# Performance work log

Measured on AMD Instinct MI355X. Metric: run time of the kernel, lower is better.

The kernel has to match this reference:

```python
import jax, jax.numpy as jnp
import numpy as np

B, T, C = 4, 2048, 1024
H, D = 16, 64  # num_heads, head_size; H*D == C


def setup_inputs() -> dict:
    key = jax.random.key(0)
    ks = jax.random.split(key, 6)
    s = C ** -0.5
    return {
        "x": jax.random.normal(ks[0], (B, T, C), dtype=jnp.float32),
        "Wq": jax.random.normal(ks[1], (H, C, D), dtype=jnp.float32) * s,
        "Wk": jax.random.normal(ks[2], (H, C, D), dtype=jnp.float32) * s,
        "Wv": jax.random.normal(ks[3], (H, C, D), dtype=jnp.float32) * s,
        "Wo": jax.random.normal(ks[4], (C, C), dtype=jnp.float32) * s,
        "bo": jnp.zeros((C,), dtype=jnp.float32),
    }


def reference(x, Wq, Wk, Wv, Wo, bo):
    # Per-head projections, vectorized over heads: [B,T,C] x [H,C,D] -> [B,H,T,D]
    q = jnp.einsum("btc,hcd->bhtd", x, Wq)
    k = jnp.einsum("btc,hcd->bhtd", x, Wk)
    v = jnp.einsum("btc,hcd->bhtd", x, Wv)
    # NOTE: original scales by n_embd**-0.5 (input channel C), not head_size.
    scale = jnp.asarray(C, x.dtype) ** -0.5
    scores = jnp.einsum("bhtd,bhsd->bhts", q, k) * scale  # [B,H,T,T]
    causal = jnp.tril(jnp.ones((T, T), dtype=bool))
    scores = jnp.where(causal, scores, jnp.asarray(-jnp.inf, x.dtype))
    attn = jax.nn.softmax(scores, axis=-1)
    out = jnp.einsum("bhts,bhsd->bhtd", attn, v)  # [B,H,T,D]
    # concat heads: [B,T,H*D] == [B,T,C]
    out = out.transpose(0, 2, 1, 3).reshape(B, T, H * D)
    return out @ Wo.T + bo
```

## Files before the change

kernel.cpp:

```cpp
#include <hip/hip_runtime.h>
#include <hip/hip_bf16.h>
#include <math.h>

#define B_ 4
#define T_ 2048
#define C_ 1024
#define H_ 16
#define D_ 64
#define BT (B_*T_)
#define BH (B_*H_)

typedef __bf16 bf16x8 __attribute__((ext_vector_type(8)));
typedef __bf16 bf16x4 __attribute__((ext_vector_type(4)));
typedef float f32x4 __attribute__((ext_vector_type(4)));
typedef unsigned short u16;
typedef u16 u16x8 __attribute__((ext_vector_type(8)));

#define GLL(g, l) __builtin_amdgcn_global_load_lds( \
    (const __attribute__((address_space(1))) unsigned int*)(g), \
    (__attribute__((address_space(3))) unsigned int*)(l), 16, 0, 0)

#define SCALE2 0.04508422f

#define SBAR()   do { asm volatile("" ::: "memory"); __builtin_amdgcn_s_barrier(); asm volatile("" ::: "memory"); } while (0)
#define WAITV(n) asm volatile("s_waitcnt vmcnt(" #n ")" ::: "memory")

__device__ __forceinline__ u16 f2b(float f) {
    union { float f; unsigned u; } v; v.f = f;
    unsigned r = v.u + 0x7fffu + ((v.u >> 16) & 1u);
    return (u16)(r >> 16);
}

__global__ __launch_bounds__(256) void prep(const float* __restrict__ x,
                                            const float* __restrict__ Wo,
                                            const float* __restrict__ Wq,
                                            const float* __restrict__ Wk,
                                            const float* __restrict__ Wv,
                                            u16* __restrict__ xbf,
                                            u16* __restrict__ wobf,
                                            u16* __restrict__ wt) {
    __shared__ u16 lds[64][72];
    int bid = blockIdx.x, tid = threadIdx.x;
    if (bid < 8192) {
        int g = bid * 256 + tid;
        float4 v = ((const float4*)x)[g];
        ushort4 o;
        o.x = f2b(v.x); o.y = f2b(v.y); o.z = f2b(v.z); o.w = f2b(v.w);
        ((ushort4*)xbf)[g] = o;
        return;
    }
    if (bid < 9216) {
        int g = (bid - 8192) * 256 + tid;
        float4 v = ((const float4*)Wo)[g];
        ushort4 o;
        o.x = f2b(v.x); o.y = f2b(v.y); o.z = f2b(v.z); o.w = f2b(v.w);
        ((ushort4*)wobf)[g] = o;
        return;
    }
    int id = bid - 9216;
    int cb = id & 15, h = (id >> 4) & 15, w = id >> 8;
    const float* W = (w == 0) ? Wq : (w == 1) ? Wk : Wv;
    float sc = (w == 0) ? SCALE2 : 1.0f;
    int c0 = cb * 64;
    {
        int col = (tid & 15) * 4;
        for (int cc = 0; cc < 4; ++cc) {
            int r = (tid >> 4) + cc * 16;
            float4 v = *(const float4*)&W[(size_t)(h * C_ + c0 + r) * D_ + col];
            lds[r][col + 0] = f2b(v.x * sc); lds[r][col + 1] = f2b(v.y * sc);
            lds[r][col + 2] = f2b(v.z * sc); lds[r][col + 3] = f2b(v.w * sc);
        }
    }
    __syncthreads();
    {
        int tcol = (tid & 7) * 8;
        for (int cc = 0; cc < 2; ++cc) {
            int d = (tid >> 3) + cc * 32;
            u16x8 t;
            for (int j = 0; j < 8; ++j) t[j] = lds[tcol + j][d];
            *(u16x8*)&wt[(((size_t)(w * H_ + h) * D_ + d) * C_) + c0 + tcol] = t;
        }
    }
}

__global__ __launch_bounds__(256) void qkv_gemm(const u16* __restrict__ xbf,
                                                const u16* __restrict__ wt,
                                                u16* __restrict__ q, u16* __restrict__ k,
                                                u16* __restrict__ vt) {
    __shared__ u16 Al[128][64];
    __shared__ u16 Bl[128][64];
    int mb = blockIdx.x, nb = blockIdx.y;
    int tid = threadIdx.x, wv = tid >> 6, lane = tid & 63, l15 = lane & 15, quad = lane >> 4;
    int rowh = (wv & 1) * 64, colh = (wv >> 1) * 64;
    f32x4 acc[4][4];
    #pragma unroll
    for (int i = 0; i < 4; ++i)
        #pragma unroll
        for (int j = 0; j < 4; ++j) acc[i][j] = (f32x4){0.f, 0.f, 0.f, 0.f};
    int lrow = lane >> 3;
    int srow = wv * 32 + lrow;
    int scol = (((lane & 7) ^ lrow)) * 8;
    const u16* agp = &xbf[(size_t)(mb * 128 + srow) * C_ + scol];
    const u16* bgp = &wt[(size_t)(nb * 128 + srow) * C_ + scol];
    int rsw = l15 & 7;
    for (int k0 = 0; k0 < C_; k0 += 64) {
        #pragma unroll
        for (int j = 0; j < 4; ++j) {
            GLL(agp + (size_t)(j * 8) * C_ + k0, &Al[wv * 32 + j * 8][0]);
            GLL(bgp + (size_t)(j * 8) * C_ + k0, &Bl[wv * 32 + j * 8][0]);
        }
        __syncthreads();
        #pragma unroll
        for (int ks = 0; ks < 2; ++ks) {
            int cbl = (((ks << 2) | quad) ^ rsw) * 8;
            bf16x8 af[4], bf[4];
            #pragma unroll
            for (int mt = 0; mt < 4; ++mt)
                af[mt] = *(const bf16x8*)&Al[rowh + mt * 16 + l15][cbl];
            #pragma unroll
            for (int nt = 0; nt < 4; ++nt)
                bf[nt] = *(const bf16x8*)&Bl[colh + nt * 16 + l15][cbl];
            #pragma unroll
            for (int mt = 0; mt < 4; ++mt)
                #pragma unroll
                for (int nt = 0; nt < 4; ++nt)
                    acc[mt][nt] = __builtin_amdgcn_mfma_f32_16x16x32_bf16(af[mt], bf[nt], acc[mt][nt], 0, 0, 0);
        }
        __syncthreads();
    }
    int bb = (mb * 128) >> 11;
    #pragma unroll
    for (int nt = 0; nt < 4; ++nt) {
        int n0 = nb * 128 + colh + nt * 16;
        int wsel = n0 >> 10, hh = (n0 >> 6) & 15, d0 = n0 & 63;
        if (wsel == 2) {
            u16* vrow = vt + ((size_t)((bb * H_ + hh) * D_) + d0 + l15) * T_;
            #pragma unroll
            for (int mt = 0; mt < 4; ++mt) {
                int tbase = ((mb * 128 + rowh + mt * 16) & (T_ - 1)) + quad * 4;
                bf16x4 w;
                #pragma unroll
                for (int r = 0; r < 4; ++r) w[r] = (__bf16)acc[mt][nt][r];
                *(bf16x4*)&vrow[tbase] = w;
            }
        } else {
            u16* op = (wsel == 0) ? q : k;
            #pragma unroll
            for (int mt = 0; mt < 4; ++mt)
                #pragma unroll
                for (int r = 0; r < 4; ++r) {
                    int m = mb * 128 + rowh + mt * 16 + quad * 4 + r;
                    int tt = m & (T_ - 1);
                    op[((size_t)(bb * H_ + hh) * T_ + tt) * D_ + d0 + l15] = f2b(acc[mt][nt][r]);
                }
        }
    }
}

__global__ __launch_bounds__(256, 2) void attn(const u16* __restrict__ q, const u16* __restrict__ kk,
                                               const u16* __restrict__ vt, u16* __restrict__ att) {
    __shared__ u16 Kl[2][64][64];
    __shared__ u16 Vl[2][64][64];
    __shared__ u16 Pl[4][32][72];
    int bh = blockIdx.x, c = 15 - blockIdx.y;
    int b = bh >> 4, h = bh & 15;
    int tid = threadIdx.x, wid = tid >> 6, lane = tid & 63, l15 = lane & 15, quad = lane >> 4;
    const u16* qbase = q + (size_t)bh * T_ * D_;
    const u16* kbase = kk + (size_t)bh * T_ * D_;
    const u16* vbase = vt + (size_t)bh * D_ * T_;
    u16* pw = &Pl[wid][0][0];
    bf16x8 ones;
    #pragma unroll
    for (int j = 0; j < 8; ++j) ones[j] = (__bf16)1.0f;
    int r8 = lane >> 3;
    int csrc = ((lane & 7) ^ r8) * 8;
    int strow = wid * 16 + r8;
    int rsw = l15 & 7;

    int R0q = c * 128 + wid * 32;
    int ktb = 2 * c + 1;
    int kmax_w = R0q >> 6;
    bf16x8 bq[2][2];
    #pragma unroll
    for (int qt = 0; qt < 2; ++qt)
        #pragma unroll
        for (int kd = 0; kd < 2; ++kd)
            bq[qt][kd] = *(const bf16x8*)&qbase[(size_t)(R0q + qt * 16 + l15) * D_ + kd * 32 + quad * 8];
    f32x4 o[4][2];
    f32x4 lacc[2];
    #pragma unroll
    for (int dt = 0; dt < 4; ++dt)
        #pragma unroll
        for (int qt = 0; qt < 2; ++qt) o[dt][qt] = (f32x4){0.f, 0.f, 0.f, 0.f};
    lacc[0] = (f32x4){0.f, 0.f, 0.f, 0.f};
    lacc[1] = (f32x4){0.f, 0.f, 0.f, 0.f};
    #pragma unroll
    for (int j = 0; j < 2; ++j) {
        GLL(kbase + (size_t)(strow + j * 8) * D_ + csrc, &Kl[0][wid * 16 + j * 8][0]);
        GLL(vbase + (size_t)(strow + j * 8) * T_ + csrc, &Vl[0][wid * 16 + j * 8][0]);
    }
    for (int kt = 0; kt <= ktb; ++kt) {
        int cur = kt & 1;
        if (kt < ktb) {
            int kn = (kt + 1) * 64;
            #pragma unroll
            for (int j = 0; j < 2; ++j) {
                GLL(kbase + (size_t)(kn + strow + j * 8) * D_ + csrc, &Kl[cur ^ 1][wid * 16 + j * 8][0]);
                GLL(vbase + (size_t)(strow + j * 8) * T_ + kn + csrc, &Vl[cur ^ 1][wid * 16 + j * 8][0]);
            }
            WAITV(4);
        } else {
            WAITV(0);
        }
        SBAR();
        if (kt <= kmax_w) {
            int k0 = kt * 64;
            f32x4 sS[4][2];
            #pragma unroll
            for (int kvt = 0; kvt < 4; ++kvt)
                #pragma unroll
                for (int qt = 0; qt < 2; ++qt) sS[kvt][qt] = (f32x4){0.f, 0.f, 0.f, 0.f};
            #pragma unroll
            for (int kd = 0; kd < 2; ++kd) {
                int cblk = (((kd << 2) | quad) ^ rsw) * 8;
                bf16x8 akf[4];
                #pragma unroll
                for (int kvt = 0; kvt < 4; ++kvt)
                    akf[kvt] = *(const bf16x8*)&Kl[cur][kvt * 16 + l15][cblk];
                #pragma unroll
                for (int kvt = 0; kvt < 4; ++kvt)
                    #pragma unroll
                    for (int qt = 0; qt < 2; ++qt)
                        sS[kvt][qt] = __builtin_amdgcn_mfma_f32_16x16x32_bf16(akf[kvt], bq[qt][kd], sS[kvt][qt], 0, 0, 0);
            }
            if (kt == kmax_w) {
                #pragma unroll
                for (int qt = 0; qt < 2; ++qt) {
                    int qabs = R0q + qt * 16 + l15;
                    #pragma unroll
                    for (int kvt = 0; kvt < 4; ++kvt) {
                        int kvb = k0 + kvt * 16 + quad * 4;
                        #pragma unroll
                        for (int r = 0; r < 4; ++r)
                            if (kvb + r > qabs) sS[kvt][qt][r] = -INFINITY;
                    }
                }
            }
            #pragma unroll
            for (int kvt = 0; kvt < 4; ++kvt)
                #pragma unroll
                for (int qt = 0; qt < 2; ++qt)
                    #pragma unroll
                    for (int r = 0; r < 4; ++r)
                        sS[kvt][qt][r] = __builtin_amdgcn_exp2f(sS[kvt][qt][r]);
            #pragma unroll
            for (int qt = 0; qt < 2; ++qt)
                #pragma unroll
                for (int kvt = 0; kvt < 4; ++kvt) {
                    bf16x4 w;
                    #pragma unroll
                    for (int r = 0; r < 4; ++r) w[r] = (__bf16)sS[kvt][qt][r];
                    *(bf16x4*)&pw[(qt * 16 + l15) * 72 + kvt * 16 + quad * 4] = w;
                }
            #pragma unroll
            for (int ks = 0; ks < 2; ++ks) {
                int cblk = (((ks << 2) | quad) ^ rsw) * 8;
                bf16x8 avf[4];
                #pragma unroll
                for (int dt = 0; dt < 4; ++dt)
                    avf[dt] = *(const bf16x8*)&Vl[cur][dt * 16 + l15][cblk];
                #pragma unroll
                for (int qt = 0; qt < 2; ++qt) {
                    bf16x8 bp = *(const bf16x8*)&pw[(qt * 16 + l15) * 72 + ks * 32 + quad * 8];
                    #pragma unroll
                    for (int dt = 0; dt < 4; ++dt)
                        o[dt][qt] = __builtin_amdgcn_mfma_f32_16x16x32_bf16(avf[dt], bp, o[dt][qt], 0, 0, 0);
                    lacc[qt] = __builtin_amdgcn_mfma_f32_16x16x32_bf16(ones, bp, lacc[qt], 0, 0, 0);
                }
            }
        }
        SBAR();
    }
    #pragma unroll
    for (int qt = 0; qt < 2; ++qt) {
        float rl = __builtin_amdgcn_rcpf(lacc[qt][0]);
        int qabs = R0q + qt * 16 + l15;
        #pragma unroll
        for (int dt = 0; dt < 4; ++dt) {
            bf16x4 w;
            #pragma unroll
            for (int r = 0; r < 4; ++r) w[r] = (__bf16)(o[dt][qt][r] * rl);
            *(bf16x4*)&att[(size_t)(b * T_ + qabs) * C_ + h * 64 + dt * 16 + quad * 4] = w;
        }
    }
}

__global__ __launch_bounds__(256) void out_gemm(const u16* __restrict__ att,
                                                const u16* __restrict__ wo,
                                                const float* __restrict__ bo,
                                                float* __restrict__ out) {
    __shared__ u16 Al[128][64];
    __shared__ u16 Bl[128][64];
    int mb = blockIdx.x, nb = blockIdx.y;
    int tid = threadIdx.x, wv = tid >> 6, lane = tid & 63, l15 = lane & 15, quad = lane >> 4;
    int rowh = (wv & 1) * 64, colh = (wv >> 1) * 64;
    f32x4 acc[4][4];
    #pragma unroll
    for (int i = 0; i < 4; ++i)
        #pragma unroll
        for (int j = 0; j < 4; ++j) acc[i][j] = (f32x4){0.f, 0.f, 0.f, 0.f};
    int lrow = lane >> 3;
    int srow = wv * 32 + lrow;
    int scol = (((lane & 7) ^ lrow)) * 8;
    const u16* agp = &att[(size_t)(mb * 128 + srow) * C_ + scol];
    const u16* bgp = &wo[(size_t)(nb * 128 + srow) * C_ + scol];
    int rsw = l15 & 7;
    for (int k0 = 0; k0 < C_; k0 += 64) {
        #pragma unroll
        for (int j = 0; j < 4; ++j) {
            GLL(agp + (size_t)(j * 8) * C_ + k0, &Al[wv * 32 + j * 8][0]);
            GLL(bgp + (size_t)(j * 8) * C_ + k0, &Bl[wv * 32 + j * 8][0]);
        }
        __syncthreads();
        #pragma unroll
        for (int ks = 0; ks < 2; ++ks) {
            int cbl = (((ks << 2) | quad) ^ rsw) * 8;
            bf16x8 af[4], bf[4];
            #pragma unroll
            for (int mt = 0; mt < 4; ++mt)
                af[mt] = *(const bf16x8*)&Al[rowh + mt * 16 + l15][cbl];
            #pragma unroll
            for (int nt = 0; nt < 4; ++nt)
                bf[nt] = *(const bf16x8*)&Bl[colh + nt * 16 + l15][cbl];
            #pragma unroll
            for (int mt = 0; mt < 4; ++mt)
                #pragma unroll
                for (int nt = 0; nt < 4; ++nt)
                    acc[mt][nt] = __builtin_amdgcn_mfma_f32_16x16x32_bf16(af[mt], bf[nt], acc[mt][nt], 0, 0, 0);
        }
        __syncthreads();
    }
    #pragma unroll
    for (int nt = 0; nt < 4; ++nt) {
        int n = nb * 128 + colh + nt * 16 + l15;
        float bias = bo[n];
        #pragma unroll
        for (int mt = 0; mt < 4; ++mt)
            #pragma unroll
            for (int r = 0; r < 4; ++r) {
                int m = mb * 128 + rowh + mt * 16 + quad * 4 + r;
                out[(size_t)m * C_ + n] = acc[mt][nt][r] + bias;
            }
    }
}

extern "C" void kernel_launch(void* const* d_in, const int* in_sizes, int n_in,
                              void* d_out, int out_size, void* d_ws, size_t ws_size,
                              hipStream_t stream) {
    const float* x  = (const float*)d_in[0];
    const float* Wq = (const float*)d_in[1];
    const float* Wk = (const float*)d_in[2];
    const float* Wv = (const float*)d_in[3];
    const float* Wo = (const float*)d_in[4];
    const float* bo = (const float*)d_in[5];
    float* out = (float*)d_out;
    char* ws = (char*)d_ws;
    u16* xbf  = (u16*)(ws + (size_t)0);
    u16* wt   = (u16*)(ws + ((size_t)16 << 20));
    u16* wobf = (u16*)(ws + ((size_t)22 << 20));
    u16* qb   = (u16*)(ws + ((size_t)24 << 20));
    u16* kb   = (u16*)(ws + ((size_t)40 << 20));
    u16* vtb  = (u16*)(ws + ((size_t)56 << 20));
    u16* attb = (u16*)(ws + ((size_t)72 << 20));

    hipLaunchKernelGGL(prep, dim3(9984), dim3(256), 0, stream, x, Wo, Wq, Wk, Wv, xbf, wobf, wt);
    hipLaunchKernelGGL(qkv_gemm, dim3(BT / 128, 3 * C_ / 128), dim3(256), 0, stream, xbf, wt, qb, kb, vtb);
    hipLaunchKernelGGL(attn, dim3(BH, 16), dim3(256), 0, stream, qb, kb, vtb, attb);
    hipLaunchKernelGGL(out_gemm, dim3(BT / 128, C_ / 128), dim3(256), 0, stream, attb, wobf, bo, out);
}
```

Baseline: 225.0 us.

## Fuse all four stages into one persistent kernel with grid barriers

```diff
diff --git a/kernel.cpp b/kernel.cpp
--- a/kernel.cpp
+++ b/kernel.cpp
@@ -9,6 +9,7 @@
 #define D_ 64
 #define BT (B_*T_)
 #define BH (B_*H_)
+#define NBLK 512u
 
 typedef __bf16 bf16x8 __attribute__((ext_vector_type(8)));
 typedef __bf16 bf16x4 __attribute__((ext_vector_type(4)));
@@ -31,326 +32,341 @@
     return (u16)(r >> 16);
 }
 
-__global__ __launch_bounds__(256) void prep(const float* __restrict__ x,
-                                            const float* __restrict__ Wo,
-                                            const float* __restrict__ Wq,
-                                            const float* __restrict__ Wk,
-                                            const float* __restrict__ Wv,
-                                            u16* __restrict__ xbf,
-                                            u16* __restrict__ wobf,
-                                            u16* __restrict__ wt) {
-    __shared__ u16 lds[64][72];
+__device__ __forceinline__ void gridbar(unsigned* cnt, int idx) {
+    __syncthreads();
+    if (threadIdx.x == 0) {
+        __threadfence();
+        atomicAdd(&cnt[idx], 1u);
+        while (__hip_atomic_load(&cnt[idx], __ATOMIC_RELAXED, __HIP_MEMORY_SCOPE_AGENT) < NBLK)
+            __builtin_amdgcn_s_sleep(2);
+        __threadfence();
+    }
+    __syncthreads();
+}
+
+union SMem {
+    struct { u16 Al[128][64]; u16 Bl[128][64]; } g;
+    struct { u16 Kl[2][64][64]; u16 Vl[2][64][64]; u16 Pl[4][32][72]; } a;
+    u16 p[64][72];
+};
+
+__global__ __launch_bounds__(256, 2) void fused(
+    const float* __restrict__ x,
+    const float* __restrict__ Wq, const float* __restrict__ Wk,
+    const float* __restrict__ Wv, const float* __restrict__ Wo,
+    const float* __restrict__ bo,
+    u16* __restrict__ xbf, u16* __restrict__ wobf, u16* __restrict__ wt,
+    u16* __restrict__ qb, u16* __restrict__ kb, u16* __restrict__ vtb,
+    u16* __restrict__ attb, float* __restrict__ out, unsigned* __restrict__ bar)
+{
+    __shared__ SMem sm;
     int bid = blockIdx.x, tid = threadIdx.x;
-    if (bid < 8192) {
-        int g = bid * 256 + tid;
-        float4 v = ((const float4*)x)[g];
-        ushort4 o;
-        o.x = f2b(v.x); o.y = f2b(v.y); o.z = f2b(v.z); o.w = f2b(v.w);
-        ((ushort4*)xbf)[g] = o;
-        return;
-    }
-    if (bid < 9216) {
-        int g = (bid - 8192) * 256 + tid;
-        float4 v = ((const float4*)Wo)[g];
-        ushort4 o;
-        o.x = f2b(v.x); o.y = f2b(v.y); o.z = f2b(v.z); o.w = f2b(v.w);
-        ((ushort4*)wobf)[g] = o;
-        return;
-    }
-    int id = bid - 9216;
-    int cb = id & 15, h = (id >> 4) & 15, w = id >> 8;
-    const float* W = (w == 0) ? Wq : (w == 1) ? Wk : Wv;
-    float sc = (w == 0) ? SCALE2 : 1.0f;
-    int c0 = cb * 64;
+    int lane = tid & 63, l15 = lane & 15, quad = lane >> 4;
+    int wv = tid >> 6;
+
+    for (int u = bid; u < 9984; u += 512) {
+        if (u < 8192) {
+            int g = u * 256 + tid;
+            float4 v = ((const float4*)x)[g];
+            ushort4 o4;
+            o4.x = f2b(v.x); o4.y = f2b(v.y); o4.z = f2b(v.z); o4.w = f2b(v.w);
+            ((ushort4*)xbf)[g] = o4;
+        } else if (u < 9216) {
+            int g = (u - 8192) * 256 + tid;
+            float4 v = ((const float4*)Wo)[g];
+            ushort4 o4;
+            o4.x = f2b(v.x); o4.y = f2b(v.y); o4.z = f2b(v.z); o4.w = f2b(v.w);
+            ((ushort4*)wobf)[g] = o4;
+        } else {
+            int id = u - 9216;
+            int cb = id & 15, h = (id >> 4) & 15, w = id >> 8;
+            const float* W = (w == 0) ? Wq : (w == 1) ? Wk : Wv;
+            float sc = (w == 0) ? SCALE2 : 1.0f;
+            int c0 = cb * 64;
+            {
+                int col = (tid & 15) * 4;
+                for (int cc = 0; cc < 4; ++cc) {
+                    int r = (tid >> 4) + cc * 16;
+                    float4 v = *(const float4*)&W[(size_t)(h * C_ + c0 + r) * D_ + col];
+                    sm.p[r][col + 0] = f2b(v.x * sc); sm.p[r][col + 1] = f2b(v.y * sc);
+                    sm.p[r][col + 2] = f2b(v.z * sc); sm.p[r][col + 3] = f2b(v.w * sc);
+                }
+            }
+            __syncthreads();
+            {
+                int tcol = (tid & 7) * 8;
+                for (int cc = 0; cc < 2; ++cc) {
+                    int d = (tid >> 3) + cc * 32;
+                    u16x8 t;
+                    for (int j = 0; j < 8; ++j) t[j] = sm.p[tcol + j][d];
+                    *(u16x8*)&wt[(((size_t)(w * H_ + h) * D_ + d) * C_) + c0 + tcol] = t;
+                }
+            }
+            __syncthreads();
+        }
+    }
+    gridbar(bar, 0);
+
     {
-        int col = (tid & 15) * 4;
-        for (int cc = 0; cc < 4; ++cc) {
-            int r = (tid >> 4) + cc * 16;
-            float4 v = *(const float4*)&W[(size_t)(h * C_ + c0 + r) * D_ + col];
-            lds[r][col + 0] = f2b(v.x * sc); lds[r][col + 1] = f2b(v.y * sc);
-            lds[r][col + 2] = f2b(v.z * sc); lds[r][col + 3] = f2b(v.w * sc);
-        }
-    }
-    __syncthreads();
+        int rowh = (wv & 1) * 64, colh = (wv >> 1) * 64;
+        int lrow = lane >> 3;
+        int srow = wv * 32 + lrow;
+        int scol = ((lane & 7) ^ lrow) * 8;
+        int rsw = l15 & 7;
+        for (int i = 0; i < 3; ++i) {
+            int u = bid + 512 * i;
+            int mb = u & 63, nb = u >> 6;
+            f32x4 acc[4][4];
+            #pragma unroll
+            for (int a1 = 0; a1 < 4; ++a1)
+                #pragma unroll
+                for (int a2 = 0; a2 < 4; ++a2) acc[a1][a2] = (f32x4){0.f, 0.f, 0.f, 0.f};
+            const u16* agp = &xbf[(size_t)(mb * 128 + srow) * C_ + scol];
+            const u16* bgp = &wt[(size_t)(nb * 128 + srow) * C_ + scol];
+            for (int k0 = 0; k0 < C_; k0 += 64) {
+                #pragma unroll
+                for (int j = 0; j < 4; ++j) {
+                    GLL(agp + (size_t)(j * 8) * C_ + k0, &sm.g.Al[wv * 32 + j * 8][0]);
+                    GLL(bgp + (size_t)(j * 8) * C_ + k0, &sm.g.Bl[wv * 32 + j * 8][0]);
+                }
+                __syncthreads();
+                #pragma unroll
+                for (int ks = 0; ks < 2; ++ks) {
+                    int cbl = (((ks << 2) | quad) ^ rsw) * 8;
+                    bf16x8 af[4], bf[4];
+                    #pragma unroll
+                    for (int mt = 0; mt < 4; ++mt)
+                        af[mt] = *(const bf16x8*)&sm.g.Al[rowh + mt * 16 + l15][cbl];
+                    #pragma unroll
+                    for (int nt = 0; nt < 4; ++nt)
+                        bf[nt] = *(const bf16x8*)&sm.g.Bl[colh + nt * 16 + l15][cbl];
+                    #pragma unroll
+                    for (int mt = 0; mt < 4; ++mt)
+                        #pragma unroll
+                        for (int nt = 0; nt < 4; ++nt)
+                            acc[mt][nt] = __builtin_amdgcn_mfma_f32_16x16x32_bf16(af[mt], bf[nt], acc[mt][nt], 0, 0, 0);
+                }
+                __syncthreads();
+            }
+            int bb = (mb * 128) >> 11;
+            #pragma unroll
+            for (int nt = 0; nt < 4; ++nt) {
+                int n0 = nb * 128 + colh + nt * 16;
+                int wsel = n0 >> 10, hh = (n0 >> 6) & 15, d0 = n0 & 63;
+                if (wsel == 2) {
+                    u16* vrow = vtb + ((size_t)((bb * H_ + hh) * D_) + d0 + l15) * T_;
+                    #pragma unroll
+                    for (int mt = 0; mt < 4; ++mt) {
+                        int tbase = ((mb * 128 + rowh + mt * 16) & (T_ - 1)) + quad * 4;
+                        bf16x4 w;
+                        #pragma unroll
+                        for (int r = 0; r < 4; ++r) w[r] = (__bf16)acc[mt][nt][r];
+                        *(bf16x4*)&vrow[tbase] = w;
+                    }
+                } else {
+                    u16* op = (wsel == 0) ? qb : kb;
+                    #pragma unroll
+                    for (int mt = 0; mt < 4; ++mt)
+                        #pragma unroll
+                        for (int r = 0; r < 4; ++r) {
+                            int m = mb * 128 + rowh + mt * 16 + quad * 4 + r;
+                            int tt = m & (T_ - 1);
+                            op[((size_t)(bb * H_ + hh) * T_ + tt) * D_ + d0 + l15] = f2b(acc[mt][nt][r]);
+                        }
+                }
+            }
+        }
+    }
+    gridbar(bar, 1);
+
     {
-        int tcol = (tid & 7) * 8;
-        for (int cc = 0; cc < 2; ++cc) {
-            int d = (tid >> 3) + cc * 32;
-            u16x8 t;
-            for (int j = 0; j < 8; ++j) t[j] = lds[tcol + j][d];
-            *(u16x8*)&wt[(((size_t)(w * H_ + h) * D_ + d) * C_) + c0 + tcol] = t;
-        }
-    }
-}
-
-__global__ __launch_bounds__(256) void qkv_gemm(const u16* __restrict__ xbf,
-                                                const u16* __restrict__ wt,
-                                                u16* __restrict__ q, u16* __restrict__ k,
-                                                u16* __restrict__ vt) {
-    __shared__ u16 Al[128][64];
-    __shared__ u16 Bl[128][64];
-    int mb = blockIdx.x, nb = blockIdx.y;
-    int tid = threadIdx.x, wv = tid >> 6, lane = tid & 63, l15 = lane & 15, quad = lane >> 4;
-    int rowh = (wv & 1) * 64, colh = (wv >> 1) * 64;
-    f32x4 acc[4][4];
-    #pragma unroll
-    for (int i = 0; i < 4; ++i)
+        int wid = wv;
+        int bh = bid & 63, y = bid >> 6;
+        int b = bh >> 4, h = bh & 15;
+        const u16* qbase = qb + (size_t)bh * T_ * D_;
+        const u16* kbase = kb + (size_t)bh * T_ * D_;
+        const u16* vbase = vtb + (size_t)bh * D_ * T_;
+        u16* pw = &sm.a.Pl[wid][0][0];
+        bf16x8 ones;
         #pragma unroll
-        for (int j = 0; j < 4; ++j) acc[i][j] = (f32x4){0.f, 0.f, 0.f, 0.f};
-    int lrow = lane >> 3;
-    int srow = wv * 32 + lrow;
-    int scol = (((lane & 7) ^ lrow)) * 8;
-    const u16* agp = &xbf[(size_t)(mb * 128 + srow) * C_ + scol];
-    const u16* bgp = &wt[(size_t)(nb * 128 + srow) * C_ + scol];
-    int rsw = l15 & 7;
-    for (int k0 = 0; k0 < C_; k0 += 64) {
+        for (int j = 0; j < 8; ++j) ones[j] = (__bf16)1.0f;
+        int r8 = lane >> 3;
+        int csrc = ((lane & 7) ^ r8) * 8;
+        int strow = wid * 16 + r8;
+        int rsw = l15 & 7;
+        for (int p = 0; p < 2; ++p) {
+            int c = p ? y : 15 - y;
+            int R0q = c * 128 + wid * 32;
+            int ktb = 2 * c + 1;
+            int kmax_w = R0q >> 6;
+            bf16x8 bq[2][2];
+            #pragma unroll
+            for (int qt = 0; qt < 2; ++qt)
+                #pragma unroll
+                for (int kd = 0; kd < 2; ++kd)
+                    bq[qt][kd] = *(const bf16x8*)&qbase[(size_t)(R0q + qt * 16 + l15) * D_ + kd * 32 + quad * 8];
+            f32x4 o[4][2];
+            f32x4 lacc[2];
+            #pragma unroll
+            for (int dt = 0; dt < 4; ++dt)
+                #pragma unroll
+                for (int qt = 0; qt < 2; ++qt) o[dt][qt] = (f32x4){0.f, 0.f, 0.f, 0.f};
+            lacc[0] = (f32x4){0.f, 0.f, 0.f, 0.f};
+            lacc[1] = (f32x4){0.f, 0.f, 0.f, 0.f};
+            #pragma unroll
+            for (int j = 0; j < 2; ++j) {
+                GLL(kbase + (size_t)(strow + j * 8) * D_ + csrc, &sm.a.Kl[0][wid * 16 + j * 8][0]);
+                GLL(vbase + (size_t)(strow + j * 8) * T_ + csrc, &sm.a.Vl[0][wid * 16 + j * 8][0]);
+            }
+            for (int kt = 0; kt <= ktb; ++kt) {
+                int cur = kt & 1;
+                if (kt < ktb) {
+                    int kn = (kt + 1) * 64;
+                    #pragma unroll
+                    for (int j = 0; j < 2; ++j) {
+                        GLL(kbase + (size_t)(kn + strow + j * 8) * D_ + csrc, &sm.a.Kl[cur ^ 1][wid * 16 + j * 8][0]);
+                        GLL(vbase + (size_t)(strow + j * 8) * T_ + kn + csrc, &sm.a.Vl[cur ^ 1][wid * 16 + j * 8][0]);
+                    }
+                    WAITV(4);
+                } else {
+                    WAITV(0);
+                }
+                SBAR();
+                if (kt <= kmax_w) {
+                    int k0 = kt * 64;
+                    f32x4 sS[4][2];
+                    #pragma unroll
+                    for (int kvt = 0; kvt < 4; ++kvt)
+                        #pragma unroll
+                        for (int qt = 0; qt < 2; ++qt) sS[kvt][qt] = (f32x4){0.f, 0.f, 0.f, 0.f};
+                    #pragma unroll
+                    for (int kd = 0; kd < 2; ++kd) {
+                        int cblk = (((kd << 2) | quad) ^ rsw) * 8;
+                        bf16x8 akf[4];
+                        #pragma unroll
+                        for (int kvt = 0; kvt < 4; ++kvt)
+                            akf[kvt] = *(const bf16x8*)&sm.a.Kl[cur][kvt * 16 + l15][cblk];
+                        #pragma unroll
+                        for (int kvt = 0; kvt < 4; ++kvt)
+                            #pragma unroll
+                            for (int qt = 0; qt < 2; ++qt)
+                                sS[kvt][qt] = __builtin_amdgcn_mfma_f32_16x16x32_bf16(akf[kvt], bq[qt][kd], sS[kvt][qt], 0, 0, 0);
+                    }
+                    if (kt == kmax_w) {
+                        #pragma unroll
+                        for (int qt = 0; qt < 2; ++qt) {
+                            int qabs = R0q + qt * 16 + l15;
+                            #pragma unroll
+                            for (int kvt = 0; kvt < 4; ++kvt) {
+                                int kvb = k0 + kvt * 16 + quad * 4;
+                                #pragma unroll
+                                for (int r = 0; r < 4; ++r)
+                                    if (kvb + r > qabs) sS[kvt][qt][r] = -INFINITY;
+                            }
+                        }
+                    }
+                    #pragma unroll
+                    for (int kvt = 0; kvt < 4; ++kvt)
+                        #pragma unroll
+                        for (int qt = 0; qt < 2; ++qt)
+                            #pragma unroll
+                            for (int r = 0; r < 4; ++r)
+                                sS[kvt][qt][r] = __builtin_amdgcn_exp2f(sS[kvt][qt][r]);
+                    #pragma unroll
+                    for (int qt = 0; qt < 2; ++qt)
+                        #pragma unroll
+                        for (int kvt = 0; kvt < 4; ++kvt) {
+                            bf16x4 w;
+                            #pragma unroll
+                            for (int r = 0; r < 4; ++r) w[r] = (__bf16)sS[kvt][qt][r];
+                            *(bf16x4*)&pw[(qt * 16 + l15) * 72 + kvt * 16 + quad * 4] = w;
+                        }
+                    #pragma unroll
+                    for (int ks = 0; ks < 2; ++ks) {
+                        int cblk = (((ks << 2) | quad) ^ rsw) * 8;
+                        bf16x8 avf[4];
+                        #pragma unroll
+                        for (int dt = 0; dt < 4; ++dt)
+                            avf[dt] = *(const bf16x8*)&sm.a.Vl[cur][dt * 16 + l15][cblk];
+                        #pragma unroll
+                        for (int qt = 0; qt < 2; ++qt) {
+                            bf16x8 bp = *(const bf16x8*)&pw[(qt * 16 + l15) * 72 + ks * 32 + quad * 8];
+                            #pragma unroll
+                            for (int dt = 0; dt < 4; ++dt)
+                                o[dt][qt] = __builtin_amdgcn_mfma_f32_16x16x32_bf16(avf[dt], bp, o[dt][qt], 0, 0, 0);
+                            lacc[qt] = __builtin_amdgcn_mfma_f32_16x16x32_bf16(ones, bp, lacc[qt], 0, 0, 0);
+                        }
+                    }
+                }
+                SBAR();
+            }
+            #pragma unroll
+            for (int qt = 0; qt < 2; ++qt) {
+                float rl = __builtin_amdgcn_rcpf(lacc[qt][0]);
+                int qabs = R0q + qt * 16 + l15;
+                #pragma unroll
+                for (int dt = 0; dt < 4; ++dt) {
+                    bf16x4 w;
+                    #pragma unroll
+                    for (int r = 0; r < 4; ++r) w[r] = (__bf16)(o[dt][qt][r] * rl);
+                    *(bf16x4*)&attb[(size_t)(b * T_ + qabs) * C_ + h * 64 + dt * 16 + quad * 4] = w;
+                }
+            }
+        }
+    }
+    gridbar(bar, 2);
+
+    {
+        int mb = bid & 63, nb = bid >> 6;
+        int rowh = (wv & 1) * 64, colh = (wv >> 1) * 64;
+        f32x4 acc[4][4];
         #pragma unroll
-        for (int j = 0; j < 4; ++j) {
-            GLL(agp + (size_t)(j * 8) * C_ + k0, &Al[wv * 32 + j * 8][0]);
-            GLL(bgp + (size_t)(j * 8) * C_ + k0, &Bl[wv * 32 + j * 8][0]);
-        }
-        __syncthreads();
+        for (int a1 = 0; a1 < 4; ++a1)
+            #pragma unroll
+            for (int a2 = 0; a2 < 4; ++a2) acc[a1][a2] = (f32x4){0.f, 0.f, 0.f, 0.f};
+        int lrow = lane >> 3;
+        int srow = wv * 32 + lrow;
+        int scol = ((lane & 7) ^ lrow) * 8;
+        const u16* agp = &attb[(size_t)(mb * 128 + srow) * C_ + scol];
+        const u16* bgp = &wobf[(size_t)(nb * 128 + srow) * C_ + scol];
+        int rsw = l15 & 7;
+        for (int k0 = 0; k0 < C_; k0 += 64) {
+            #pragma unroll
+            for (int j = 0; j < 4; ++j) {
+                GLL(agp + (size_t)(j * 8) * C_ + k0, &sm.g.Al[wv * 32 + j * 8][0]);
+                GLL(bgp + (size_t)(j * 8) * C_ + k0, &sm.g.Bl[wv * 32 + j * 8][0]);
+            }
+            __syncthreads();
+            #pragma unroll
+            for (int ks = 0; ks < 2; ++ks) {
+                int cbl = (((ks << 2) | quad) ^ rsw) * 8;
+                bf16x8 af[4], bf[4];
+                #pragma unroll
+                for (int mt = 0; mt < 4; ++mt)
+                    af[mt] = *(const bf16x8*)&sm.g.Al[rowh + mt * 16 + l15][cbl];
+                #pragma unroll
+                for (int nt = 0; nt < 4; ++nt)
+                    bf[nt] = *(const bf16x8*)&sm.g.Bl[colh + nt * 16 + l15][cbl];
+                #pragma unroll
+                for (int mt = 0; mt < 4; ++mt)
+                    #pragma unroll
+                    for (int nt = 0; nt < 4; ++nt)
+                        acc[mt][nt] = __builtin_amdgcn_mfma_f32_16x16x32_bf16(af[mt], bf[nt], acc[mt][nt], 0, 0, 0);
+            }
+            __syncthreads();
+        }
         #pragma unroll
-        for (int ks = 0; ks < 2; ++ks) {
-            int cbl = (((ks << 2) | quad) ^ rsw) * 8;
-            bf16x8 af[4], bf[4];
-            #pragma unroll
-            for (int mt = 0; mt < 4; ++mt)
-                af[mt] = *(const bf16x8*)&Al[rowh + mt * 16 + l15][cbl];
-            #pragma unroll
-            for (int nt = 0; nt < 4; ++nt)
-                bf[nt] = *(const bf16x8*)&Bl[colh + nt * 16 + l15][cbl];
-            #pragma unroll
-            for (int mt = 0; mt < 4; ++mt)
-                #pragma unroll
-                for (int nt = 0; nt < 4; ++nt)
-                    acc[mt][nt] = __builtin_amdgcn_mfma_f32_16x16x32_bf16(af[mt], bf[nt], acc[mt][nt], 0, 0, 0);
-        }
-        __syncthreads();
-    }
-    int bb = (mb * 128) >> 11;
-    #pragma unroll
-    for (int nt = 0; nt < 4; ++nt) {
-        int n0 = nb * 128 + colh + nt * 16;
-        int wsel = n0 >> 10, hh = (n0 >> 6) & 15, d0 = n0 & 63;
-        if (wsel == 2) {
-            u16* vrow = vt + ((size_t)((bb * H_ + hh) * D_) + d0 + l15) * T_;
-            #pragma unroll
-            for (int mt = 0; mt < 4; ++mt) {
-                int tbase = ((mb * 128 + rowh + mt * 16) & (T_ - 1)) + quad * 4;
-                bf16x4 w;
-                #pragma unroll
-                for (int r = 0; r < 4; ++r) w[r] = (__bf16)acc[mt][nt][r];
-                *(bf16x4*)&vrow[tbase] = w;
-            }
-        } else {
-            u16* op = (wsel == 0) ? q : k;
+        for (int nt = 0; nt < 4; ++nt) {
+            int n = nb * 128 + colh + nt * 16 + l15;
+            float bias = bo[n];
             #pragma unroll
             for (int mt = 0; mt < 4; ++mt)
                 #pragma unroll
                 for (int r = 0; r < 4; ++r) {
                     int m = mb * 128 + rowh + mt * 16 + quad * 4 + r;
-                    int tt = m & (T_ - 1);
-                    op[((size_t)(bb * H_ + hh) * T_ + tt) * D_ + d0 + l15] = f2b(acc[mt][nt][r]);
-                }
-        }
-    }
-}
-
-__global__ __launch_bounds__(256, 2) void attn(const u16* __restrict__ q, const u16* __restrict__ kk,
-                                               const u16* __restrict__ vt, u16* __restrict__ att) {
-    __shared__ u16 Kl[2][64][64];
-    __shared__ u16 Vl[2][64][64];
-    __shared__ u16 Pl[4][32][72];
-    int bh = blockIdx.x, c = 15 - blockIdx.y;
-    int b = bh >> 4, h = bh & 15;
-    int tid = threadIdx.x, wid = tid >> 6, lane = tid & 63, l15 = lane & 15, quad = lane >> 4;
-    const u16* qbase = q + (size_t)bh * T_ * D_;
-    const u16* kbase = kk + (size_t)bh * T_ * D_;
-    const u16* vbase = vt + (size_t)bh * D_ * T_;
-    u16* pw = &Pl[wid][0][0];
-    bf16x8 ones;
-    #pragma unroll
-    for (int j = 0; j < 8; ++j) ones[j] = (__bf16)1.0f;
-    int r8 = lane >> 3;
-    int csrc = ((lane & 7) ^ r8) * 8;
-    int strow = wid * 16 + r8;
-    int rsw = l15 & 7;
-
-    int R0q = c * 128 + wid * 32;
-    int ktb = 2 * c + 1;
-    int kmax_w = R0q >> 6;
-    bf16x8 bq[2][2];
-    #pragma unroll
-    for (int qt = 0; qt < 2; ++qt)
-        #pragma unroll
-        for (int kd = 0; kd < 2; ++kd)
-            bq[qt][kd] = *(const bf16x8*)&qbase[(size_t)(R0q + qt * 16 + l15) * D_ + kd * 32 + quad * 8];
-    f32x4 o[4][2];
-    f32x4 lacc[2];
-    #pragma unroll
-    for (int dt = 0; dt < 4; ++dt)
-        #pragma unroll
-        for (int qt = 0; qt < 2; ++qt) o[dt][qt] = (f32x4){0.f, 0.f, 0.f, 0.f};
-    lacc[0] = (f32x4){0.f, 0.f, 0.f, 0.f};
-    lacc[1] = (f32x4){0.f, 0.f, 0.f, 0.f};
-    #pragma unroll
-    for (int j = 0; j < 2; ++j) {
-        GLL(kbase + (size_t)(strow + j * 8) * D_ + csrc, &Kl[0][wid * 16 + j * 8][0]);
-        GLL(vbase + (size_t)(strow + j * 8) * T_ + csrc, &Vl[0][wid * 16 + j * 8][0]);
-    }
-    for (int kt = 0; kt <= ktb; ++kt) {
-        int cur = kt & 1;
-        if (kt < ktb) {
-            int kn = (kt + 1) * 64;
-            #pragma unroll
-            for (int j = 0; j < 2; ++j) {
-                GLL(kbase + (size_t)(kn + strow + j * 8) * D_ + csrc, &Kl[cur ^ 1][wid * 16 + j * 8][0]);
-                GLL(vbase + (size_t)(strow + j * 8) * T_ + kn + csrc, &Vl[cur ^ 1][wid * 16 + j * 8][0]);
-            }
-            WAITV(4);
-        } else {
-            WAITV(0);
-        }
-        SBAR();
-        if (kt <= kmax_w) {
-            int k0 = kt * 64;
-            f32x4 sS[4][2];
-            #pragma unroll
-            for (int kvt = 0; kvt < 4; ++kvt)
-                #pragma unroll
-                for (int qt = 0; qt < 2; ++qt) sS[kvt][qt] = (f32x4){0.f, 0.f, 0.f, 0.f};
-            #pragma unroll
-            for (int kd = 0; kd < 2; ++kd) {
-                int cblk = (((kd << 2) | quad) ^ rsw) * 8;
-                bf16x8 akf[4];
-                #pragma unroll
-                for (int kvt = 0; kvt < 4; ++kvt)
-                    akf[kvt] = *(const bf16x8*)&Kl[cur][kvt * 16 + l15][cblk];
-                #pragma unroll
-                for (int kvt = 0; kvt < 4; ++kvt)
-                    #pragma unroll
-                    for (int qt = 0; qt < 2; ++qt)
-                        sS[kvt][qt] = __builtin_amdgcn_mfma_f32_16x16x32_bf16(akf[kvt], bq[qt][kd], sS[kvt][qt], 0, 0, 0);
-            }
-            if (kt == kmax_w) {
-                #pragma unroll
-                for (int qt = 0; qt < 2; ++qt) {
-                    int qabs = R0q + qt * 16 + l15;
-                    #pragma unroll
-                    for (int kvt = 0; kvt < 4; ++kvt) {
-                        int kvb = k0 + kvt * 16 + quad * 4;
-                        #pragma unroll
-                        for (int r = 0; r < 4; ++r)
-                            if (kvb + r > qabs) sS[kvt][qt][r] = -INFINITY;
-                    }
-                }
-            }
-            #pragma unroll
-            for (int kvt = 0; kvt < 4; ++kvt)
-                #pragma unroll
-                for (int qt = 0; qt < 2; ++qt)
-                    #pragma unroll
-                    for (int r = 0; r < 4; ++r)
-                        sS[kvt][qt][r] = __builtin_amdgcn_exp2f(sS[kvt][qt][r]);
-            #pragma unroll
-            for (int qt = 0; qt < 2; ++qt)
-                #pragma unroll
-                for (int kvt = 0; kvt < 4; ++kvt) {
-                    bf16x4 w;
-                    #pragma unroll
-                    for (int r = 0; r < 4; ++r) w[r] = (__bf16)sS[kvt][qt][r];
-                    *(bf16x4*)&pw[(qt * 16 + l15) * 72 + kvt * 16 + quad * 4] = w;
-                }
-            #pragma unroll
-            for (int ks = 0; ks < 2; ++ks) {
-                int cblk = (((ks << 2) | quad) ^ rsw) * 8;
-                bf16x8 avf[4];
-                #pragma unroll
-                for (int dt = 0; dt < 4; ++dt)
-                    avf[dt] = *(const bf16x8*)&Vl[cur][dt * 16 + l15][cblk];
-                #pragma unroll
-                for (int qt = 0; qt < 2; ++qt) {
-                    bf16x8 bp = *(const bf16x8*)&pw[(qt * 16 + l15) * 72 + ks * 32 + quad * 8];
-                    #pragma unroll
-                    for (int dt = 0; dt < 4; ++dt)
-                        o[dt][qt] = __builtin_amdgcn_mfma_f32_16x16x32_bf16(avf[dt], bp, o[dt][qt], 0, 0, 0);
-                    lacc[qt] = __builtin_amdgcn_mfma_f32_16x16x32_bf16(ones, bp, lacc[qt], 0, 0, 0);
-                }
-            }
-        }
-        SBAR();
-    }
-    #pragma unroll
-    for (int qt = 0; qt < 2; ++qt) {
-        float rl = __builtin_amdgcn_rcpf(lacc[qt][0]);
-        int qabs = R0q + qt * 16 + l15;
-        #pragma unroll
-        for (int dt = 0; dt < 4; ++dt) {
-            bf16x4 w;
-            #pragma unroll
-            for (int r = 0; r < 4; ++r) w[r] = (__bf16)(o[dt][qt][r] * rl);
-            *(bf16x4*)&att[(size_t)(b * T_ + qabs) * C_ + h * 64 + dt * 16 + quad * 4] = w;
-        }
-    }
-}
-
-__global__ __launch_bounds__(256) void out_gemm(const u16* __restrict__ att,
-                                                const u16* __restrict__ wo,
-                                                const float* __restrict__ bo,
-                                                float* __restrict__ out) {
-    __shared__ u16 Al[128][64];
-    __shared__ u16 Bl[128][64];
-    int mb = blockIdx.x, nb = blockIdx.y;
-    int tid = threadIdx.x, wv = tid >> 6, lane = tid & 63, l15 = lane & 15, quad = lane >> 4;
-    int rowh = (wv & 1) * 64, colh = (wv >> 1) * 64;
-    f32x4 acc[4][4];
-    #pragma unroll
-    for (int i = 0; i < 4; ++i)
-        #pragma unroll
-        for (int j = 0; j < 4; ++j) acc[i][j] = (f32x4){0.f, 0.f, 0.f, 0.f};
-    int lrow = lane >> 3;
-    int srow = wv * 32 + lrow;
-    int scol = (((lane & 7) ^ lrow)) * 8;
-    const u16* agp = &att[(size_t)(mb * 128 + srow) * C_ + scol];
-    const u16* bgp = &wo[(size_t)(nb * 128 + srow) * C_ + scol];
-    int rsw = l15 & 7;
-    for (int k0 = 0; k0 < C_; k0 += 64) {
-        #pragma unroll
-        for (int j = 0; j < 4; ++j) {
-            GLL(agp + (size_t)(j * 8) * C_ + k0, &Al[wv * 32 + j * 8][0]);
-            GLL(bgp + (size_t)(j * 8) * C_ + k0, &Bl[wv * 32 + j * 8][0]);
-        }
-        __syncthreads();
-        #pragma unroll
-        for (int ks = 0; ks < 2; ++ks) {
-            int cbl = (((ks << 2) | quad) ^ rsw) * 8;
-            bf16x8 af[4], bf[4];
-            #pragma unroll
-            for (int mt = 0; mt < 4; ++mt)
-                af[mt] = *(const bf16x8*)&Al[rowh + mt * 16 + l15][cbl];
-            #pragma unroll
-            for (int nt = 0; nt < 4; ++nt)
-                bf[nt] = *(const bf16x8*)&Bl[colh + nt * 16 + l15][cbl];
-            #pragma unroll
-            for (int mt = 0; mt < 4; ++mt)
-                #pragma unroll
-                for (int nt = 0; nt < 4; ++nt)
-                    acc[mt][nt] = __builtin_amdgcn_mfma_f32_16x16x32_bf16(af[mt], bf[nt], acc[mt][nt], 0, 0, 0);
-        }
-        __syncthreads();
-    }
-    #pragma unroll
-    for (int nt = 0; nt < 4; ++nt) {
-        int n = nb * 128 + colh + nt * 16 + l15;
-        float bias = bo[n];
-        #pragma unroll
-        for (int mt = 0; mt < 4; ++mt)
-            #pragma unroll
-            for (int r = 0; r < 4; ++r) {
-                int m = mb * 128 + rowh + mt * 16 + quad * 4 + r;
-                out[(size_t)m * C_ + n] = acc[mt][nt][r] + bias;
-            }
+                    out[(size_t)m * C_ + n] = acc[mt][nt][r] + bias;
+                }
+        }
     }
 }
 
@@ -372,9 +388,9 @@
     u16* kb   = (u16*)(ws + ((size_t)40 << 20));
     u16* vtb  = (u16*)(ws + ((size_t)56 << 20));
     u16* attb = (u16*)(ws + ((size_t)72 << 20));
-
-    hipLaunchKernelGGL(prep, dim3(9984), dim3(256), 0, stream, x, Wo, Wq, Wk, Wv, xbf, wobf, wt);
-    hipLaunchKernelGGL(qkv_gemm, dim3(BT / 128, 3 * C_ / 128), dim3(256), 0, stream, xbf, wt, qb, kb, vtb);
-    hipLaunchKernelGGL(attn, dim3(BH, 16), dim3(256), 0, stream, qb, kb, vtb, attb);
-    hipLaunchKernelGGL(out_gemm, dim3(BT / 128, C_ / 128), dim3(256), 0, stream, attb, wobf, bo, out);
+    unsigned* bar = (unsigned*)(ws + ((size_t)88 << 20));
+
+    hipMemsetAsync(bar, 0, 16, stream);
+    hipLaunchKernelGGL(fused, dim3(NBLK), dim3(256), 0, stream,
+                       x, Wq, Wk, Wv, Wo, bo, xbf, wobf, wt, qb, kb, vtb, attb, out, bar);
 }
```

Measured after the change: 405.2 us. 80.1% more time.
